# Optimization experiments

Measured on AMD Instinct MI355X. Metric: run time of the kernel, lower is better.

Reference implementation:

```python
import jax, jax.numpy as jnp
import numpy as np

N, E = 20000, 320000
IN, OUT, H1, H2 = 256, 32, 8, 1
NEG_SLOPE = 0.2


def _gatv2(x, src, dst, Wsrc, bsrc, Wdst, bdst, attn, Wres, bres, heads, dout):
    n = x.shape[0]
    fs = (x @ Wsrc + bsrc).reshape(n, heads, dout)   # (N,H,D)
    fd = (x @ Wdst + bdst).reshape(n, heads, dout)   # (N,H,D)
    # GATv2: leaky_relu BEFORE the attention dot product
    e = jax.nn.leaky_relu(fs[src] + fd[dst], NEG_SLOPE)      # (E,H,D)
    logits = jnp.einsum('ehd,hd->eh', e, attn)               # (E,H)
    # edge softmax over destination-node segments
    m = jax.ops.segment_max(logits, dst, num_segments=n)     # (N,H)
    ex = jnp.exp(logits - m[dst])
    s = jax.ops.segment_sum(ex, dst, num_segments=n)         # (N,H)
    alpha = ex / s[dst]                                      # (E,H)
    msg = alpha[:, :, None] * fs[src]                        # (E,H,D)
    out = jax.ops.segment_sum(msg, dst, num_segments=n)      # (N,H,D)
    res = (x @ Wres + bres).reshape(n, heads, dout)          # residual (dims differ -> Linear)
    return out + res


def setup_inputs() -> dict:
    key = jax.random.key(0)
    ks = jax.random.split(key, 16)
    sc = lambda fin: 1.0 / np.sqrt(fin)
    d = {}
    d['x'] = jax.random.normal(ks[0], (N, IN), jnp.float32)
    d['src'] = jax.random.randint(ks[1], (E,), 0, N, jnp.int32)
    d['dst'] = jax.random.randint(ks[2], (E,), 0, N, jnp.int32)
    # layer 1: IN -> OUT*H1
    d['Wsrc1'] = jax.random.normal(ks[3], (IN, OUT * H1), jnp.float32) * sc(IN)
    d['bsrc1'] = jnp.zeros((OUT * H1,), jnp.float32)
    d['Wdst1'] = jax.random.normal(ks[4], (IN, OUT * H1), jnp.float32) * sc(IN)
    d['bdst1'] = jnp.zeros((OUT * H1,), jnp.float32)
    d['attn1'] = jax.random.normal(ks[5], (H1, OUT), jnp.float32) * sc(OUT)
    d['Wres1'] = jax.random.normal(ks[6], (IN, OUT * H1), jnp.float32) * sc(IN)
    d['bres1'] = jnp.zeros((OUT * H1,), jnp.float32)
    # layer 2: OUT*H1 -> OUT, 1 head
    D2 = OUT * H1
    d['Wsrc2'] = jax.random.normal(ks[7], (D2, OUT * H2), jnp.float32) * sc(D2)
    d['bsrc2'] = jnp.zeros((OUT * H2,), jnp.float32)
    d['Wdst2'] = jax.random.normal(ks[8], (D2, OUT * H2), jnp.float32) * sc(D2)
    d['bdst2'] = jnp.zeros((OUT * H2,), jnp.float32)
    d['attn2'] = jax.random.normal(ks[9], (H2, OUT), jnp.float32) * sc(OUT)
    d['Wres2'] = jax.random.normal(ks[10], (D2, OUT * H2), jnp.float32) * sc(D2)
    d['bres2'] = jnp.zeros((OUT * H2,), jnp.float32)
    return d


def reference(x, src, dst,
              Wsrc1, bsrc1, Wdst1, bdst1, attn1, Wres1, bres1,
              Wsrc2, bsrc2, Wdst2, bdst2, attn2, Wres2, bres2):
    y = _gatv2(x, src, dst, Wsrc1, bsrc1, Wdst1, bdst1, attn1, Wres1, bres1, H1, OUT)
    y = jax.nn.relu(y)                       # (N, 8, OUT)
    y = y.reshape(x.shape[0], -1)            # (N, 8*OUT)
    y = _gatv2(y, src, dst, Wsrc2, bsrc2, Wdst2, bdst2, attn2, Wres2, bres2, H2, OUT)
    return y                                  # (N, 1, OUT)
```

## Files before the change

### kernel.cpp

```cpp
#include <hip/hip_runtime.h>
#include <hip/hip_bf16.h>

#define N_NODES 20000
#define N_PAD   20096
#define N_EDGES 320000
#define D_IN    256
#define NEG     0.2f
#define MAXDEG  64

typedef __attribute__((ext_vector_type(8))) short short8;
typedef __attribute__((ext_vector_type(4))) float f32x4;
typedef __attribute__((ext_vector_type(4))) unsigned short u16x4;

__device__ __forceinline__ unsigned short f2b(float f) {
    unsigned int u = __float_as_uint(f);
    unsigned int r = (u + 0x7FFFu + ((u >> 16) & 1u)) >> 16;
    return (unsigned short)r;
}
__device__ __forceinline__ float b2f(unsigned short u) {
    union { unsigned int i; float f; } v;
    v.i = ((unsigned int)u) << 16;
    return v.f;
}

__device__ __forceinline__ void gload16(const void* g, void* l) {
    __builtin_amdgcn_global_load_lds((const __attribute__((address_space(1))) void*)g,
                                     (__attribute__((address_space(3))) void*)l, 16, 0, 0);
}

#define PB1 2512
#define PB2 3280
#define PB3 3376
#define PB4 3455
#define PREP_BLOCKS 3503
__global__ __launch_bounds__(256) void k_prep(
    const float* __restrict__ x, unsigned short* __restrict__ xb,
    const float* __restrict__ Ws1, const float* __restrict__ Wd1, const float* __restrict__ Wr1,
    unsigned short* __restrict__ wt,
    const float* __restrict__ Ws2, const float* __restrict__ Wd2, const float* __restrict__ Wr2,
    unsigned short* __restrict__ wt2,
    int* __restrict__ cnt, unsigned short* __restrict__ yb)
{
    int bid = blockIdx.x, tid = threadIdx.x;
    if (bid < PB1) {
        int i = bid * 256 + tid;
        int row = i >> 5, c8 = (i & 31) * 8;
        short8 v = {0, 0, 0, 0, 0, 0, 0, 0};
        if (row < N_NODES) {
            float4 a = *reinterpret_cast<const float4*>(x + (size_t)row * 256 + c8);
            float4 b = *reinterpret_cast<const float4*>(x + (size_t)row * 256 + c8 + 4);
            v[0] = (short)f2b(a.x); v[1] = (short)f2b(a.y); v[2] = (short)f2b(a.z); v[3] = (short)f2b(a.w);
            v[4] = (short)f2b(b.x); v[5] = (short)f2b(b.y); v[6] = (short)f2b(b.z); v[7] = (short)f2b(b.w);
        }
        *reinterpret_cast<short8*>(xb + (size_t)row * 256 + c8) = v;
    } else if (bid < PB2) {
        int n = bid - PB1, k = tid;
        const float* W = (n < 256) ? Ws1 : ((n < 512) ? Wd1 : Wr1);
        int c = n & 255;
        wt[(size_t)n * 256 + k] = f2b(W[(size_t)k * 256 + c]);
    } else if (bid < PB3) {
        int n = bid - PB2, k = tid;
        const float* W = (n < 32) ? Ws2 : ((n < 64) ? Wd2 : Wr2);
        int c = n & 31;
        wt2[(size_t)n * 256 + (k ^ ((n & 7) << 3))] = f2b(W[(size_t)k * 32 + c]);
    } else if (bid < PB4) {
        int idx = (bid - PB3) * 256 + tid;
        if (idx < N_NODES) cnt[idx] = 0;
    } else {
        int j = (bid - PB4) * 256 + tid;
        ((unsigned int*)(yb + (size_t)N_NODES * 256))[j] = 0u;
    }
}

#define GEMM1_BLOCKS 942
#define BUCKET_BLOCKS 1250
__global__ __launch_bounds__(256) void k_gemm_l1_mfma(
    const unsigned short* __restrict__ xb,
    const unsigned short* __restrict__ wt,
    const float* __restrict__ bs, const float* __restrict__ bd, const float* __restrict__ br,
    unsigned short* __restrict__ fs, unsigned short* __restrict__ fd, unsigned short* __restrict__ res,
    const int* __restrict__ src, const int* __restrict__ dst,
    int* __restrict__ cnt, int* __restrict__ colp)
{
    __shared__ __align__(16) unsigned short SH[128 * 64];
    unsigned short* As = SH;
    unsigned short* Bs = SH + 128 * 32;
    int t = threadIdx.x;
    int bid = blockIdx.x;

    if (bid >= GEMM1_BLOCKS) {
        int e = (bid - GEMM1_BLOCKS) * 256 + t;
        if (e < N_EDGES) {
            int d = dst[e];
            int pos = atomicAdd(&cnt[d], 1);
            if (pos < MAXDEG) colp[d * MAXDEG + pos] = src[e];
        }
        return;
    }

    int lane = t & 63, w = t >> 6;
    const int q = 117, r = 6;
    int xcd = bid & 7, slot = bid >> 3;
    int wg = (xcd < r ? xcd * (q + 1) : r * (q + 1) + (xcd - r) * q) + slot;
    int mb = wg / 6, nb = wg % 6;
    int row0 = mb * 128;
    int which = nb >> 1;
    int col0 = (nb & 1) * 128;
    int ncol0 = nb * 128;
    unsigned short* out = (which == 0) ? fs : ((which == 1) ? fd : res);
    const float* bias   = (which == 0) ? bs : ((which == 1) ? bd : br);
    int wr = w >> 1, wc = w & 1;

    f32x4 acc[4][4] = {};

    for (int k0 = 0; k0 < 256; k0 += 32) {
        if (k0) __syncthreads();
#pragma unroll
        for (int rnd = 0; rnd < 2; rnd++) {
            int c = rnd * 256 + t;
            int row = c >> 2, kc = (c & 3) * 8;
            gload16(xb + (size_t)(row0 + row) * 256 + k0 + kc, (char*)As + c * 16);
            gload16(wt + (size_t)(ncol0 + row) * 256 + k0 + kc, (char*)Bs + c * 16);
        }
        __syncthreads();
        short8 a[4], b[4];
#pragma unroll
        for (int m = 0; m < 4; m++)
            a[m] = *reinterpret_cast<const short8*>((const char*)As + ((wr * 64 + m * 16 + (lane & 15)) * 64 + (lane >> 4) * 16));
#pragma unroll
        for (int n = 0; n < 4; n++)
            b[n] = *reinterpret_cast<const short8*>((const char*)Bs + ((wc * 64 + n * 16 + (lane & 15)) * 64 + (lane >> 4) * 16));
#pragma unroll
        for (int m = 0; m < 4; m++)
#pragma unroll
            for (int n = 0; n < 4; n++)
                acc[m][n] = __builtin_amdgcn_mfma_f32_16x16x32_bf16(a[m], b[n], acc[m][n], 0, 0, 0);
    }

    int cgrp = lane >> 4, ccol = lane & 15;
    float bvals[4];
#pragma unroll
    for (int n = 0; n < 4; n++) bvals[n] = bias[col0 + wc * 64 + n * 16 + ccol];

#pragma unroll
    for (int p = 0; p < 2; p++) {
        __syncthreads();
        if (wr == p) {
#pragma unroll
            for (int m = 0; m < 4; m++)
#pragma unroll
                for (int n = 0; n < 4; n++)
#pragma unroll
                    for (int q2 = 0; q2 < 4; q2++) {
                        int lr = m * 16 + cgrp * 4 + q2;
                        int cb = (wc * 64 + n * 16 + ccol) * 2;
                        int addr = lr * 256 + (cb ^ (((lr >> 2) & 3) << 5));
                        *(unsigned short*)((char*)SH + addr) = f2b(acc[m][n][q2] + bvals[n]);
                    }
        }
        __syncthreads();
#pragma unroll
        for (int it = 0; it < 4; it++) {
            int lr = it * 16 + (t >> 4);
            int cb = (t & 15) * 16;
            short8 v = *(const short8*)((const char*)SH + (lr * 256 + (cb ^ (((lr >> 2) & 3) << 5))));
            int gr = row0 + p * 64 + lr;
            if (gr < N_NODES)
                *reinterpret_cast<short8*>(out + (size_t)gr * 256 + col0 + (t & 15) * 8) = v;
        }
    }
}

__global__ __launch_bounds__(64) void k_gather_l1(
    const int* __restrict__ cnt, const int* __restrict__ colp,
    const unsigned short* __restrict__ fs1, const unsigned short* __restrict__ fd1,
    const unsigned short* __restrict__ res1, const float* __restrict__ attn1,
    unsigned short* __restrict__ y)
{
    int n = blockIdx.x;
    int l = threadIdx.x;
    u16x4 fdv4 = *reinterpret_cast<const u16x4*>(fd1 + (size_t)n * 256 + l * 4);
    float fdv[4] = {b2f(fdv4[0]), b2f(fdv4[1]), b2f(fdv4[2]), b2f(fdv4[3])};
    float4 attv = *reinterpret_cast<const float4*>(attn1 + l * 4);
    float att[4] = {attv.x, attv.y, attv.z, attv.w};

    const int* colrow = colp + (size_t)n * MAXDEG;
    int deg = cnt[n];
    if (deg > MAXDEG) deg = MAXDEG;

    float m = -1e30f, s = 0.f;
    float acc[4] = {0.f, 0.f, 0.f, 0.f};
    int c0 = (0 < deg) ? colrow[0] : 0;
    int c1 = (1 < deg) ? colrow[1] : 0;
    u16x4 f0 = *reinterpret_cast<const u16x4*>(fs1 + (size_t)c0 * 256 + l * 4);
    u16x4 f1 = *reinterpret_cast<const u16x4*>(fs1 + (size_t)c1 * 256 + l * 4);
    for (int idx = 0; idx < deg; ++idx) {
        u16x4 fv4 = f0;
        f0 = f1;
        int c2 = (idx + 2 < deg) ? colrow[idx + 2] : 0;
        f1 = *reinterpret_cast<const u16x4*>(fs1 + (size_t)c2 * 256 + l * 4);
        float fv[4] = {b2f(fv4[0]), b2f(fv4[1]), b2f(fv4[2]), b2f(fv4[3])};
        float t0 = fv[0] + fdv[0]; t0 = t0 > 0.f ? t0 : NEG * t0;
        float t1 = fv[1] + fdv[1]; t1 = t1 > 0.f ? t1 : NEG * t1;
        float t2 = fv[2] + fdv[2]; t2 = t2 > 0.f ? t2 : NEG * t2;
        float t3 = fv[3] + fdv[3]; t3 = t3 > 0.f ? t3 : NEG * t3;
        float p = t0 * att[0] + t1 * att[1] + t2 * att[2] + t3 * att[3];
        p += __shfl_xor(p, 1);
        p += __shfl_xor(p, 2);
        p += __shfl_xor(p, 4);
        float mn = fmaxf(m, p);
        float e  = __expf(p - mn);
        float sc = __expf(m - mn);
        s = s * sc + e;
        acc[0] = acc[0] * sc + e * fv[0];
        acc[1] = acc[1] * sc + e * fv[1];
        acc[2] = acc[2] * sc + e * fv[2];
        acc[3] = acc[3] * sc + e * fv[3];
        m = mn;
    }
    u16x4 rv4 = *reinterpret_cast<const u16x4*>(res1 + (size_t)n * 256 + l * 4);
    float inv = (s > 0.f) ? 1.f / s : 0.f;
    u16x4 o;
    o[0] = f2b(fmaxf(acc[0] * inv + b2f(rv4[0]), 0.f));
    o[1] = f2b(fmaxf(acc[1] * inv + b2f(rv4[1]), 0.f));
    o[2] = f2b(fmaxf(acc[2] * inv + b2f(rv4[2]), 0.f));
    o[3] = f2b(fmaxf(acc[3] * inv + b2f(rv4[3]), 0.f));
    *reinterpret_cast<u16x4*>(y + (size_t)n * 256 + l * 4) = o;
}

__global__ __launch_bounds__(256) void k_gemm_l2_mfma(
    const unsigned short* __restrict__ yb,
    const unsigned short* __restrict__ wt2,
    const float* __restrict__ bs, const float* __restrict__ bd, const float* __restrict__ br,
    unsigned short* __restrict__ fs2, unsigned short* __restrict__ fd2, unsigned short* __restrict__ res2)
{
    __shared__ __align__(16) unsigned short Bs[96 * 256];
    __shared__ __align__(16) unsigned short As[128 * 32];
    int t = threadIdx.x;
    int lane = t & 63, w = t >> 6;
    int row0 = blockIdx.x * 128;

#pragma unroll
    for (int i = 0; i < 12; i++) {
        int c = i * 256 + t;
        gload16(wt2 + (size_t)c * 8, (char*)Bs + (size_t)c * 16);
    }

    f32x4 acc[2][6] = {};
    int arow0 = w * 32;

    for (int k0 = 0; k0 < 256; k0 += 32) {
        if (k0) __syncthreads();
        {
            int c0 = t, c1 = 256 + t;
            gload16(yb + (size_t)(row0 + (c0 >> 2)) * 256 + k0 + (c0 & 3) * 8, (char*)As + c0 * 16);
            gload16(yb + (size_t)(row0 + (c1 >> 2)) * 256 + k0 + (c1 & 3) * 8, (char*)As + c1 * 16);
        }
        __syncthreads();
        short8 a[2], b[6];
#pragma unroll
        for (int m = 0; m < 2; m++)
            a[m] = *reinterpret_cast<const short8*>((const char*)As + ((arow0 + m * 16 + (lane & 15)) * 64 + (lane >> 4) * 16));
#pragma unroll
        for (int n = 0; n < 6; n++) {
            int brow = n * 16 + (lane & 15);
            int kbyte = (k0 + (lane >> 4) * 8) * 2;
            b[n] = *reinterpret_cast<const short8*>((const char*)Bs + (brow * 512 + (kbyte ^ ((brow & 7) << 4))));
        }
#pragma unroll
        for (int m = 0; m < 2; m++)
#pragma unroll
            for (int n = 0; n < 6; n++)
                acc[m][n] = __builtin_amdgcn_mfma_f32_16x16x32_bf16(a[m], b[n], acc[m][n], 0, 0, 0);
    }

    int cgrp = lane >> 4, ccol = lane & 15;
#pragma unroll
    for (int n = 0; n < 6; n++) {
        int which = n >> 1;
        int cc = (n & 1) * 16 + ccol;
        unsigned short* out = (which == 0) ? fs2 : ((which == 1) ? fd2 : res2);
        const float* bias   = (which == 0) ? bs  : ((which == 1) ? bd  : br);
        float bv = bias[cc];
#pragma unroll
        for (int m = 0; m < 2; m++) {
            int rbase = row0 + arow0 + m * 16 + cgrp * 4;
#pragma unroll
            for (int q2 = 0; q2 < 4; q2++) {
                int rr = rbase + q2;
                if (rr < N_NODES) out[(size_t)rr * 32 + cc] = f2b(acc[m][n][q2] + bv);
            }
        }
    }
}

__global__ __launch_bounds__(64) void k_gather_l2(
    const int* __restrict__ cnt, const int* __restrict__ colp,
    const unsigned short* __restrict__ fs2, const unsigned short* __restrict__ fd2,
    const unsigned short* __restrict__ res2, const float* __restrict__ attn2,
    float* __restrict__ out)
{
    int n = blockIdx.x;
    int l = threadIdx.x;
    int d = l & 31, h = l >> 5;
    float fdv = b2f(fd2[(size_t)n * 32 + d]);
    float att = attn2[d];
    const int* colrow = colp + (size_t)n * MAXDEG;
    int deg = cnt[n];
    if (deg > MAXDEG) deg = MAXDEG;

    float m = -1e30f, s = 0.f, acc = 0.f;
    int c0 = (h < deg) ? colrow[h] : 0;
    float fv_next = b2f(fs2[(size_t)c0 * 32 + d]);
    for (int i = h; i < deg; i += 2) {
        float fv = fv_next;
        int cn = (i + 2 < deg) ? colrow[i + 2] : 0;
        fv_next = b2f(fs2[(size_t)cn * 32 + d]);
        float t0 = fv + fdv; t0 = t0 > 0.f ? t0 : NEG * t0;
        float p = t0 * att;
        p += __shfl_xor(p, 1);
        p += __shfl_xor(p, 2);
        p += __shfl_xor(p, 4);
        p += __shfl_xor(p, 8);
        p += __shfl_xor(p, 16);
        float mn = fmaxf(m, p);
        float e  = __expf(p - mn);
        float sc = __expf(m - mn);
        s = s * sc + e;
        acc = acc * sc + e * fv;
        m = mn;
    }
    float mo = __shfl_xor(m, 32);
    float mstar = fmaxf(m, mo);
    float myc = __expf(m - mstar);
    float sp = s * myc, ap = acc * myc;
    float st = sp + __shfl_xor(sp, 32);
    float at = ap + __shfl_xor(ap, 32);
    if (l < 32) {
        float rv = b2f(res2[(size_t)n * 32 + d]);
        float inv = (st > 0.f) ? 1.f / st : 0.f;
        out[(size_t)n * 32 + d] = at * inv + rv;
    }
}

extern "C" void kernel_launch(void* const* d_in, const int* in_sizes, int n_in,
                              void* d_out, int out_size, void* d_ws, size_t ws_size,
                              hipStream_t stream)
{
    const float* x   = (const float*)d_in[0];
    const int*   src = (const int*)d_in[1];
    const int*   dst = (const int*)d_in[2];
    const float* Ws1 = (const float*)d_in[3];
    const float* bs1 = (const float*)d_in[4];
    const float* Wd1 = (const float*)d_in[5];
    const float* bd1 = (const float*)d_in[6];
    const float* at1 = (const float*)d_in[7];
    const float* Wr1 = (const float*)d_in[8];
    const float* br1 = (const float*)d_in[9];
    const float* Ws2 = (const float*)d_in[10];
    const float* bs2 = (const float*)d_in[11];
    const float* Wd2 = (const float*)d_in[12];
    const float* bd2 = (const float*)d_in[13];
    const float* at2 = (const float*)d_in[14];
    const float* Wr2 = (const float*)d_in[15];
    const float* br2 = (const float*)d_in[16];
    float* out = (float*)d_out;

    char* w = (char*)d_ws;
    size_t off = 0;
    auto alloc = [&](size_t bytes) { void* p = w + off; off += (bytes + 255) & ~(size_t)255; return p; };
    int*   cnt    = (int*)  alloc((size_t)N_NODES * 4);
    int*   colp   = (int*)  alloc((size_t)N_NODES * MAXDEG * 4);
    unsigned short* fs1 = (unsigned short*)alloc((size_t)N_NODES * 256 * 2);
    unsigned short* fd1 = (unsigned short*)alloc((size_t)N_NODES * 256 * 2);
    unsigned short* res1= (unsigned short*)alloc((size_t)N_NODES * 256 * 2);
    unsigned short* fs2 = (unsigned short*)alloc((size_t)N_NODES * 32 * 2);
    unsigned short* fd2 = (unsigned short*)alloc((size_t)N_NODES * 32 * 2);
    unsigned short* res2= (unsigned short*)alloc((size_t)N_NODES * 32 * 2);
    unsigned short* xb  = (unsigned short*)alloc((size_t)N_PAD * 256 * 2);
    unsigned short* yb  = (unsigned short*)alloc((size_t)N_PAD * 256 * 2);
    unsigned short* wt  = (unsigned short*)alloc((size_t)768 * 256 * 2);
    unsigned short* wt2 = (unsigned short*)alloc((size_t)96 * 256 * 2);
    (void)ws_size; (void)in_sizes; (void)n_in; (void)out_size;

    k_prep<<<PREP_BLOCKS, 256, 0, stream>>>(x, xb, Ws1, Wd1, Wr1, wt, Ws2, Wd2, Wr2, wt2,
                                            cnt, yb);
    k_gemm_l1_mfma<<<GEMM1_BLOCKS + BUCKET_BLOCKS, 256, 0, stream>>>(
        xb, wt, bs1, bd1, br1, fs1, fd1, res1, src, dst, cnt, colp);
    k_gather_l1<<<N_NODES, 64, 0, stream>>>(cnt, colp, fs1, fd1, res1, at1, yb);
    k_gemm_l2_mfma<<<N_PAD / 128, 256, 0, stream>>>(yb, wt2, bs2, bd2, br2, fs2, fd2, res2);
    k_gather_l2<<<N_NODES, 64, 0, stream>>>(cnt, colp, fs2, fd2, res2, at2, out);
}
```

Baseline: 113.0 us.

## Double-buffer LDS tiles in both GEMMs and halve layer-2 row tile

Both MFMA GEMM kernels now use two LDS buffers, so the global-to-LDS load for the next K slice is issued before the current slice's MFMAs, with a single barrier per iteration. The aim is to hide global load latency behind compute. Layer 2 also shrinks its row tile from 128 to 64, which doubles the block count (about 157 to 314) for better CU occupancy but reloads the full weight panel into LDS in twice as many blocks. Layer 1's LDS use doubles to 32KB, which may lower occupancy.

```diff
diff --git a/kernel.cpp b/kernel.cpp
--- a/kernel.cpp
+++ b/kernel.cpp
@@ -82,9 +82,7 @@
     const int* __restrict__ src, const int* __restrict__ dst,
     int* __restrict__ cnt, int* __restrict__ colp)
 {
-    __shared__ __align__(16) unsigned short SH[128 * 64];
-    unsigned short* As = SH;
-    unsigned short* Bs = SH + 128 * 32;
+    __shared__ __align__(16) unsigned short SH[2 * 128 * 64];
     int t = threadIdx.x;
     int bid = blockIdx.x;
 
@@ -111,30 +109,41 @@
     const float* bias   = (which == 0) ? bs : ((which == 1) ? bd : br);
     int wr = w >> 1, wc = w & 1;
 
-    f32x4 acc[4][4] = {};
-
-    for (int k0 = 0; k0 < 256; k0 += 32) {
-        if (k0) __syncthreads();
+    auto stage = [&](int buf, int k0) {
 #pragma unroll
         for (int rnd = 0; rnd < 2; rnd++) {
             int c = rnd * 256 + t;
             int row = c >> 2, kc = (c & 3) * 8;
-            gload16(xb + (size_t)(row0 + row) * 256 + k0 + kc, (char*)As + c * 16);
-            gload16(wt + (size_t)(ncol0 + row) * 256 + k0 + kc, (char*)Bs + c * 16);
-        }
-        __syncthreads();
+            char* base = (char*)SH + buf * 16384;
+            gload16(xb + (size_t)(row0 + row) * 256 + k0 + kc, base + c * 16);
+            gload16(wt + (size_t)(ncol0 + row) * 256 + k0 + kc, base + 8192 + c * 16);
+        }
+    };
+
+    f32x4 acc[4][4] = {};
+
+    stage(0, 0);
+    __syncthreads();
+    int cur = 0;
+#pragma unroll
+    for (int it = 0; it < 8; ++it) {
+        if (it < 7) stage(cur ^ 1, (it + 1) * 32);
+        const char* Ab = (const char*)SH + cur * 16384;
+        const char* Bb = Ab + 8192;
         short8 a[4], b[4];
 #pragma unroll
         for (int m = 0; m < 4; m++)
-            a[m] = *reinterpret_cast<const short8*>((const char*)As + ((wr * 64 + m * 16 + (lane & 15)) * 64 + (lane >> 4) * 16));
+            a[m] = *reinterpret_cast<const short8*>(Ab + ((wr * 64 + m * 16 + (lane & 15)) * 64 + (lane >> 4) * 16));
 #pragma unroll
         for (int n = 0; n < 4; n++)
-            b[n] = *reinterpret_cast<const short8*>((const char*)Bs + ((wc * 64 + n * 16 + (lane & 15)) * 64 + (lane >> 4) * 16));
+            b[n] = *reinterpret_cast<const short8*>(Bb + ((wc * 64 + n * 16 + (lane & 15)) * 64 + (lane >> 4) * 16));
 #pragma unroll
         for (int m = 0; m < 4; m++)
 #pragma unroll
             for (int n = 0; n < 4; n++)
                 acc[m][n] = __builtin_amdgcn_mfma_f32_16x16x32_bf16(a[m], b[n], acc[m][n], 0, 0, 0);
+        __syncthreads();
+        cur ^= 1;
     }
 
     int cgrp = lane >> 4, ccol = lane & 15;
@@ -144,7 +153,7 @@
 
 #pragma unroll
     for (int p = 0; p < 2; p++) {
-        __syncthreads();
+        if (p) __syncthreads();
         if (wr == p) {
 #pragma unroll
             for (int m = 0; m < 4; m++)
@@ -235,43 +244,45 @@
     unsigned short* __restrict__ fs2, unsigned short* __restrict__ fd2, unsigned short* __restrict__ res2)
 {
     __shared__ __align__(16) unsigned short Bs[96 * 256];
-    __shared__ __align__(16) unsigned short As[128 * 32];
+    __shared__ __align__(16) unsigned short As[2][64 * 32];
     int t = threadIdx.x;
     int lane = t & 63, w = t >> 6;
-    int row0 = blockIdx.x * 128;
+    int row0 = blockIdx.x * 64;
+
+    auto stage_a = [&](int buf, int k0) {
+        int c = t;
+        int row = c >> 2, kc = (c & 3) * 8;
+        gload16(yb + (size_t)(row0 + row) * 256 + k0 + kc, (char*)As[buf] + c * 16);
+    };
 
 #pragma unroll
     for (int i = 0; i < 12; i++) {
         int c = i * 256 + t;
         gload16(wt2 + (size_t)c * 8, (char*)Bs + (size_t)c * 16);
     }
-
-    f32x4 acc[2][6] = {};
-    int arow0 = w * 32;
-
-    for (int k0 = 0; k0 < 256; k0 += 32) {
-        if (k0) __syncthreads();
-        {
-            int c0 = t, c1 = 256 + t;
-            gload16(yb + (size_t)(row0 + (c0 >> 2)) * 256 + k0 + (c0 & 3) * 8, (char*)As + c0 * 16);
-            gload16(yb + (size_t)(row0 + (c1 >> 2)) * 256 + k0 + (c1 & 3) * 8, (char*)As + c1 * 16);
-        }
-        __syncthreads();
-        short8 a[2], b[6];
-#pragma unroll
-        for (int m = 0; m < 2; m++)
-            a[m] = *reinterpret_cast<const short8*>((const char*)As + ((arow0 + m * 16 + (lane & 15)) * 64 + (lane >> 4) * 16));
+    stage_a(0, 0);
+    __syncthreads();
+
+    f32x4 acc[6] = {};
+    int arow0 = w * 16;
+    int cur = 0;
+
+#pragma unroll
+    for (int it = 0; it < 8; ++it) {
+        if (it < 7) stage_a(cur ^ 1, (it + 1) * 32);
+        short8 a = *reinterpret_cast<const short8*>((const char*)As[cur] + ((arow0 + (lane & 15)) * 64 + (lane >> 4) * 16));
+        short8 b[6];
 #pragma unroll
         for (int n = 0; n < 6; n++) {
             int brow = n * 16 + (lane & 15);
-            int kbyte = (k0 + (lane >> 4) * 8) * 2;
+            int kbyte = (it * 32 + (lane >> 4) * 8) * 2;
             b[n] = *reinterpret_cast<const short8*>((const char*)Bs + (brow * 512 + (kbyte ^ ((brow & 7) << 4))));
         }
 #pragma unroll
-        for (int m = 0; m < 2; m++)
-#pragma unroll
-            for (int n = 0; n < 6; n++)
-                acc[m][n] = __builtin_amdgcn_mfma_f32_16x16x32_bf16(a[m], b[n], acc[m][n], 0, 0, 0);
+        for (int n = 0; n < 6; n++)
+            acc[n] = __builtin_amdgcn_mfma_f32_16x16x32_bf16(a, b[n], acc[n], 0, 0, 0);
+        __syncthreads();
+        cur ^= 1;
     }
 
     int cgrp = lane >> 4, ccol = lane & 15;
@@ -282,14 +293,11 @@
         unsigned short* out = (which == 0) ? fs2 : ((which == 1) ? fd2 : res2);
         const float* bias   = (which == 0) ? bs  : ((which == 1) ? bd  : br);
         float bv = bias[cc];
-#pragma unroll
-        for (int m = 0; m < 2; m++) {
-            int rbase = row0 + arow0 + m * 16 + cgrp * 4;
-#pragma unroll
-            for (int q2 = 0; q2 < 4; q2++) {
-                int rr = rbase + q2;
-                if (rr < N_NODES) out[(size_t)rr * 32 + cc] = f2b(acc[m][n][q2] + bv);
-            }
+        int rbase = row0 + arow0 + cgrp * 4;
+#pragma unroll
+        for (int q2 = 0; q2 < 4; q2++) {
+            int rr = rbase + q2;
+            if (rr < N_NODES) out[(size_t)rr * 32 + cc] = f2b(acc[n][q2] + bv);
         }
     }
 }
@@ -388,6 +396,6 @@
     k_gemm_l1_mfma<<<GEMM1_BLOCKS + BUCKET_BLOCKS, 256, 0, stream>>>(
         xb, wt, bs1, bd1, br1, fs1, fd1, res1, src, dst, cnt, colp);
     k_gather_l1<<<N_NODES, 64, 0, stream>>>(cnt, colp, fs1, fd1, res1, at1, yb);
-    k_gemm_l2_mfma<<<N_PAD / 128, 256, 0, stream>>>(yb, wt2, bs2, bd2, br2, fs2, fd2, res2);
+    k_gemm_l2_mfma<<<N_PAD / 64, 256, 0, stream>>>(yb, wt2, bs2, bd2, br2, fs2, fd2, res2);
     k_gather_l2<<<N_NODES, 64, 0, stream>>>(cnt, colp, fs2, fd2, res2, at2, out);
 }
```

Result: no change. 112.6 us (-0.4%).
